# Kernel optimization log

Hardware: AMD Instinct MI355X
Metric: run time of the kernel (lower is better)

The kernel has to match this reference:

```python
import jax, jax.numpy as jnp
import numpy as np


def setup_inputs() -> dict:
    key = jax.random.key(0)
    k1, k2 = jax.random.split(key)
    B, C, D, H, W = 2, 2, 160, 160, 160
    src = jax.random.normal(k1, (B, C, D, H, W), dtype=jnp.float32)
    # displacement field in voxel units (a few voxels, typical for registration)
    flow = jax.random.normal(k2, (B, 3, D, H, W), dtype=jnp.float32) * 2.0
    return {"src": src, "flow": flow}


def reference(src, flow):
    # SpatialTransformer.forward for the 3D case.
    # grid + flow, normalized to [-1,1] (align_corners=True), permuted, then
    # grid_sample(align_corners=True, mode='bilinear', padding_mode='zeros').
    # With align_corners=True the normalize/un-normalize round-trip is exact,
    # so the sample location is simply grid + flow in voxel coords (d,h,w).
    B, C, D, H, W = src.shape
    dt = src.dtype
    gz, gy, gx = jnp.meshgrid(
        jnp.arange(D, dtype=dt), jnp.arange(H, dtype=dt), jnp.arange(W, dtype=dt),
        indexing="ij")
    z = gz[None] + flow[:, 0]  # [B,D,H,W]
    y = gy[None] + flow[:, 1]
    x = gx[None] + flow[:, 2]

    z0 = jnp.floor(z); y0 = jnp.floor(y); x0 = jnp.floor(x)
    fz = z - z0; fy = y - y0; fx = x - x0
    z0i = z0.astype(jnp.int32); y0i = y0.astype(jnp.int32); x0i = x0.astype(jnp.int32)

    src_flat = src.reshape(B, C, D * H * W)
    out = jnp.zeros((B, C, D, H, W), dtype=dt)
    for dz in (0, 1):
        wz = fz if dz else (1.0 - fz)
        zi = z0i + dz
        for dy in (0, 1):
            wy = fy if dy else (1.0 - fy)
            yi = y0i + dy
            for dx in (0, 1):
                wx = fx if dx else (1.0 - fx)
                xi = x0i + dx
                # zeros padding: out-of-range corners contribute 0
                valid = ((zi >= 0) & (zi < D) & (yi >= 0) & (yi < H)
                         & (xi >= 0) & (xi < W))
                zc = jnp.clip(zi, 0, D - 1)
                yc = jnp.clip(yi, 0, H - 1)
                xc = jnp.clip(xi, 0, W - 1)
                idx = (zc * H + yc) * W + xc  # [B,D,H,W]
                val = jnp.take_along_axis(
                    src_flat, idx.reshape(B, 1, -1), axis=2
                ).reshape(B, C, D, H, W)
                w = (wz * wy * wx) * valid.astype(dt)  # [B,D,H,W]
                out = out + w[:, None] * val
    return out
```

## Files before the change

### kernel.cpp

```cpp
#include <hip/hip_runtime.h>


constexpr int Bv = 2, Cv = 2, Dv = 160, Hv = 160, Wv = 160;
constexpr int V = Dv * Hv * Wv;
constexpr int TOTAL = Bv * V;
constexpr size_t WS_NEEDED = (size_t)Bv * V * sizeof(float4);

__global__ __launch_bounds__(256) void pack_kernel(
    const float* __restrict__ src,
    float4* __restrict__ staged)
{
    int i = blockIdx.x * blockDim.x + threadIdx.x;
    if (i >= TOTAL) return;
    int b = i / V;
    int s = i - b * V;
    int x = s % Wv;

    const float* s0 = src + (size_t)b * Cv * V;
    const float* s1 = s0 + V;

    float c00 = s0[s], c10 = s1[s];
    float c01 = 0.f, c11 = 0.f;
    if (x < Wv - 1) { c01 = s0[s + 1]; c11 = s1[s + 1]; }
    staged[i] = make_float4(c00, c10, c01, c11);
}

__global__ __launch_bounds__(256) void warp3d_packed(
    const float4* __restrict__ staged,
    const float* __restrict__ flow,
    float* __restrict__ out)
{
    int i = blockIdx.x * blockDim.x + threadIdx.x;
    if (i >= TOTAL) return;

    int b = i / V;
    int s = i - b * V;
    int x = s % Wv;
    int t = s / Wv;
    int y = t % Hv;
    int z = t / Hv;

    const float* fb = flow + (size_t)b * 3 * V;
    float pz = (float)z + fb[s];
    float py = (float)y + fb[s + V];
    float px = (float)x + fb[s + 2 * V];

    float z0f = floorf(pz), y0f = floorf(py), x0f = floorf(px);
    float fz = pz - z0f, fy = py - y0f, fx = px - x0f;
    int z0 = (int)z0f, y0 = (int)y0f, x0 = (int)x0f;

    bool vx0 = (unsigned)x0 < (unsigned)Wv;
    bool vx1 = (unsigned)(x0 + 1) < (unsigned)Wv;
    bool lowx = (x0 < 0);
    int xc = min(max(x0, 0), Wv - 1);
    float wx0 = vx0 ? (1.f - fx) : 0.f;
    float wx1 = vx1 ? fx : 0.f;

    int zc0 = min(max(z0, 0), Dv - 1);
    int zc1 = min(max(z0 + 1, 0), Dv - 1);
    int yc0 = min(max(y0, 0), Hv - 1);
    int yc1 = min(max(y0 + 1, 0), Hv - 1);
    bool vz0 = (unsigned)z0 < (unsigned)Dv;
    bool vz1 = (unsigned)(z0 + 1) < (unsigned)Dv;
    bool vy0 = (unsigned)y0 < (unsigned)Hv;
    bool vy1 = (unsigned)(y0 + 1) < (unsigned)Hv;
    float wz0 = vz0 ? (1.f - fz) : 0.f;
    float wz1 = vz1 ? fz : 0.f;
    float wy0 = vy0 ? (1.f - fy) : 0.f;
    float wy1 = vy1 ? fy : 0.f;

    int row0 = zc0 * Hv;
    int row1 = zc1 * Hv;
    int idx00 = (row0 + yc0) * Wv + xc;
    int idx01 = (row0 + yc1) * Wv + xc;
    int idx10 = (row1 + yc0) * Wv + xc;
    int idx11 = (row1 + yc1) * Wv + xc;

    const float4* sb = staged + (size_t)b * V;
    float4 q00 = sb[idx00];
    float4 q01 = sb[idx01];
    float4 q10 = sb[idx10];
    float4 q11 = sb[idx11];

    float acc0 = 0.f, acc1 = 0.f;
    {
        float w = wz0 * wy0, a0 = w * wx0, a1 = w * wx1;
        float v1c0 = lowx ? q00.x : q00.z;
        float v1c1 = lowx ? q00.y : q00.w;
        acc0 = fmaf(a0, q00.x, fmaf(a1, v1c0, acc0));
        acc1 = fmaf(a0, q00.y, fmaf(a1, v1c1, acc1));
    }
    {
        float w = wz0 * wy1, a0 = w * wx0, a1 = w * wx1;
        float v1c0 = lowx ? q01.x : q01.z;
        float v1c1 = lowx ? q01.y : q01.w;
        acc0 = fmaf(a0, q01.x, fmaf(a1, v1c0, acc0));
        acc1 = fmaf(a0, q01.y, fmaf(a1, v1c1, acc1));
    }
    {
        float w = wz1 * wy0, a0 = w * wx0, a1 = w * wx1;
        float v1c0 = lowx ? q10.x : q10.z;
        float v1c1 = lowx ? q10.y : q10.w;
        acc0 = fmaf(a0, q10.x, fmaf(a1, v1c0, acc0));
        acc1 = fmaf(a0, q10.y, fmaf(a1, v1c1, acc1));
    }
    {
        float w = wz1 * wy1, a0 = w * wx0, a1 = w * wx1;
        float v1c0 = lowx ? q11.x : q11.z;
        float v1c1 = lowx ? q11.y : q11.w;
        acc0 = fmaf(a0, q11.x, fmaf(a1, v1c0, acc0));
        acc1 = fmaf(a0, q11.y, fmaf(a1, v1c1, acc1));
    }

    size_t ob = (size_t)b * Cv * V;
    out[ob + s]     = acc0;
    out[ob + V + s] = acc1;
}

__global__ __launch_bounds__(256) void warp3d_direct(
    const float* __restrict__ src,
    const float* __restrict__ flow,
    float* __restrict__ out)
{
    int i = blockIdx.x * blockDim.x + threadIdx.x;
    if (i >= TOTAL) return;

    int b = i / V;
    int s = i - b * V;
    int x = s % Wv;
    int t = s / Wv;
    int y = t % Hv;
    int z = t / Hv;

    const float* fb = flow + (size_t)b * 3 * V;
    float pz = (float)z + fb[s];
    float py = (float)y + fb[s + V];
    float px = (float)x + fb[s + 2 * V];

    float z0f = floorf(pz), y0f = floorf(py), x0f = floorf(px);
    float fz = pz - z0f, fy = py - y0f, fx = px - x0f;
    int z0 = (int)z0f, y0 = (int)y0f, x0 = (int)x0f;

    const float* s0 = src + (size_t)b * Cv * V;
    const float* s1 = s0 + V;

    float acc0 = 0.f, acc1 = 0.f;
    #pragma unroll
    for (int dz = 0; dz < 2; ++dz) {
        int zi = z0 + dz;
        bool vz = (unsigned)zi < (unsigned)Dv;
        float wz = dz ? fz : (1.0f - fz);
        #pragma unroll
        for (int dy = 0; dy < 2; ++dy) {
            int yi = y0 + dy;
            bool vy = (unsigned)yi < (unsigned)Hv;
            float wy = dy ? fy : (1.0f - fy);
            #pragma unroll
            for (int dx = 0; dx < 2; ++dx) {
                int xi = x0 + dx;
                bool vx = (unsigned)xi < (unsigned)Wv;
                float wx = dx ? fx : (1.0f - fx);
                if (vz & vy & vx) {
                    int idx = (zi * Hv + yi) * Wv + xi;
                    float w = wz * wy * wx;
                    acc0 = fmaf(w, s0[idx], acc0);
                    acc1 = fmaf(w, s1[idx], acc1);
                }
            }
        }
    }

    size_t ob = (size_t)b * Cv * V;
    out[ob + s]     = acc0;
    out[ob + V + s] = acc1;
}

extern "C" void kernel_launch(void* const* d_in, const int* in_sizes, int n_in,
                              void* d_out, int out_size, void* d_ws, size_t ws_size,
                              hipStream_t stream) {
    const float* src  = (const float*)d_in[0];
    const float* flow = (const float*)d_in[1];
    float* out = (float*)d_out;

    int block = 256;
    int grid = (TOTAL + block - 1) / block;

    if (ws_size >= WS_NEEDED && d_ws != nullptr) {
        float4* staged = (float4*)d_ws;
        pack_kernel<<<grid, block, 0, stream>>>(src, staged);
        warp3d_packed<<<grid, block, 0, stream>>>(staged, flow, out);
    } else {
        warp3d_direct<<<grid, block, 0, stream>>>(src, flow, out);
    }
}
```

Measured before the change: 381.8 us.

## Tile warp kernel into 3D blocks with XCD-aware mapping and vectorize packing

The gather kernel now gives each workgroup a 32x4x2 voxel tile instead of a linear 256-voxel strip. Workgroup IDs are remapped so that neighbouring tiles land on the same XCD, which is meant to improve L2 reuse of the staged neighbourhood gathers. The pack kernel now has each thread process four x-positions with float4 loads and emits four interleaved float4s, which cuts per-thread overhead. The remap assumes that NWG divides evenly by 8 and that the hardware dispatches workgroups round-robin across XCDs.

```diff
diff --git a/kernel.cpp b/kernel.cpp
--- a/kernel.cpp
+++ b/kernel.cpp
@@ -6,23 +6,39 @@
 constexpr int TOTAL = Bv * V;
 constexpr size_t WS_NEEDED = (size_t)Bv * V * sizeof(float4);
 
-__global__ __launch_bounds__(256) void pack_kernel(
+constexpr int TX = 32, TY = 4, TZ = 2;
+constexpr int NTX = Wv / TX;
+constexpr int NTY = Hv / TY;
+constexpr int NTZ = Dv / TZ;
+constexpr int TILES_PER_B = NTX * NTY * NTZ;
+constexpr int NWG = Bv * TILES_PER_B;
+constexpr int NXCD = 8;
+constexpr int CHUNK = NWG / NXCD;
+
+__global__ __launch_bounds__(256) void pack_kernel4(
     const float* __restrict__ src,
     float4* __restrict__ staged)
 {
     int i = blockIdx.x * blockDim.x + threadIdx.x;
-    if (i >= TOTAL) return;
-    int b = i / V;
-    int s = i - b * V;
-    int x = s % Wv;
+    if (i >= TOTAL / 4) return;
+    int b = i / (V / 4);
+    int s4 = (i - b * (V / 4)) * 4;
+    int x = s4 % Wv;
 
     const float* s0 = src + (size_t)b * Cv * V;
     const float* s1 = s0 + V;
 
-    float c00 = s0[s], c10 = s1[s];
-    float c01 = 0.f, c11 = 0.f;
-    if (x < Wv - 1) { c01 = s0[s + 1]; c11 = s1[s + 1]; }
-    staged[i] = make_float4(c00, c10, c01, c11);
+    float4 a0 = *(const float4*)(s0 + s4);
+    float4 a1 = *(const float4*)(s1 + s4);
+    bool last = (x + 4 >= Wv);
+    float b0 = last ? 0.f : s0[s4 + 4];
+    float b1 = last ? 0.f : s1[s4 + 4];
+
+    float4* o = staged + (size_t)b * V + s4;
+    o[0] = make_float4(a0.x, a1.x, a0.y, a1.y);
+    o[1] = make_float4(a0.y, a1.y, a0.z, a1.z);
+    o[2] = make_float4(a0.z, a1.z, a0.w, a1.w);
+    o[3] = make_float4(a0.w, a1.w, b0, b1);
 }
 
 __global__ __launch_bounds__(256) void warp3d_packed(
@@ -30,15 +46,21 @@
     const float* __restrict__ flow,
     float* __restrict__ out)
 {
-    int i = blockIdx.x * blockDim.x + threadIdx.x;
-    if (i >= TOTAL) return;
-
-    int b = i / V;
-    int s = i - b * V;
-    int x = s % Wv;
-    int t = s / Wv;
-    int y = t % Hv;
-    int z = t / Hv;
+    int bid = blockIdx.x;
+    int bt = (bid & (NXCD - 1)) * CHUNK + (bid >> 3);
+
+    int b = bt / TILES_PER_B;
+    int r = bt - b * TILES_PER_B;
+    int tix = r % NTX;
+    int t2 = r / NTX;
+    int tiy = t2 % NTY;
+    int tiz = t2 / NTY;
+
+    int tid = threadIdx.x;
+    int x = tix * TX + (tid & (TX - 1));
+    int y = tiy * TY + ((tid >> 5) & (TY - 1));
+    int z = tiz * TZ + (tid >> 7);
+    int s = (z * Hv + y) * Wv + x;
 
     const float* fb = flow + (size_t)b * 3 * V;
     float pz = (float)z + fb[s];
@@ -182,14 +204,13 @@
     const float* flow = (const float*)d_in[1];
     float* out = (float*)d_out;
 
-    int block = 256;
-    int grid = (TOTAL + block - 1) / block;
-
     if (ws_size >= WS_NEEDED && d_ws != nullptr) {
         float4* staged = (float4*)d_ws;
-        pack_kernel<<<grid, block, 0, stream>>>(src, staged);
-        warp3d_packed<<<grid, block, 0, stream>>>(staged, flow, out);
+        int packThreads = TOTAL / 4;
+        pack_kernel4<<<(packThreads + 255) / 256, 256, 0, stream>>>(src, staged);
+        warp3d_packed<<<NWG, 256, 0, stream>>>(staged, flow, out);
     } else {
-        warp3d_direct<<<grid, block, 0, stream>>>(src, flow, out);
-    }
-}
+        int grid = (TOTAL + 255) / 256;
+        warp3d_direct<<<grid, 256, 0, stream>>>(src, flow, out);
+    }
+}
```

Result: no change. 378.2 us (-0.9%).
